# Optimization experiments

Hardware: AMD Instinct MI355X
Metric: run time of the kernel (lower is better)

The kernel has to match this reference:

```python
import jax, jax.numpy as jnp
import numpy as np

D_MODEL = 2048
N_HEADS = 16
HEAD_DIM = D_MODEL // N_HEADS  # 128
ROPE_BASE = 10000.0


def _rope_cos_sin(T, hd, dtype):
    inv_freq = 1.0 / (ROPE_BASE ** (jnp.arange(0, hd, 2, dtype=jnp.float32) / hd))
    freqs = jnp.arange(T, dtype=jnp.float32)[:, None] * inv_freq[None, :]  # [T, hd/2]
    emb = jnp.concatenate([freqs, freqs], axis=-1)  # [T, hd]
    return jnp.cos(emb).astype(dtype), jnp.sin(emb).astype(dtype)


def _rotate_half(x):
    h = x.shape[-1] // 2
    return jnp.concatenate([-x[..., h:], x[..., :h]], axis=-1)


def setup_inputs() -> dict:
    key = jax.random.key(0)
    k1, k2, k3, k4 = jax.random.split(key, 4)
    B, T = 2, 2048
    x = jax.random.normal(k1, (B, T, D_MODEL), dtype=jnp.float32)
    # Linear weights stored as [in, out] so y = x @ W (same math as torch's x @ W.T)
    Wqkv = jax.random.normal(k2, (D_MODEL, 3 * D_MODEL), dtype=jnp.float32) * (D_MODEL ** -0.5)
    Wproj = jax.random.normal(k3, (D_MODEL, D_MODEL), dtype=jnp.float32) * (D_MODEL ** -0.5)
    bproj = jax.random.normal(k4, (D_MODEL,), dtype=jnp.float32) * 0.01
    # additive causal mask: 0 on/below diagonal, -1e9 above
    causal = jnp.tril(jnp.ones((T, T), dtype=bool))
    mask = jnp.where(causal, 0.0, -1e9).astype(jnp.float32)
    return {"x": x, "Wqkv": Wqkv, "Wproj": Wproj, "bproj": bproj, "mask": mask}


def reference(x, Wqkv, Wproj, bproj, mask):
    B, T, D = x.shape
    H, hd = N_HEADS, HEAD_DIM
    scale = hd ** -0.5

    qkv = x @ Wqkv  # [B, T, 3D]
    q, k, v = jnp.split(qkv, 3, axis=-1)
    q = q.reshape(B, T, H, hd).transpose(0, 2, 1, 3)  # [B, H, T, hd]
    k = k.reshape(B, T, H, hd).transpose(0, 2, 1, 3)
    v = v.reshape(B, T, H, hd).transpose(0, 2, 1, 3)

    cos, sin = _rope_cos_sin(T, hd, x.dtype)  # [T, hd]
    q = q * cos + _rotate_half(q) * sin
    k = k * cos + _rotate_half(k) * sin

    attn = jnp.einsum('bhtd,bhsd->bhts', q, k) * scale  # [B, H, T, T]
    attn = attn + mask  # broadcast [T, T] over (B, H)
    attn = jax.nn.softmax(attn, axis=-1)
    out = jnp.einsum('bhts,bhsd->bhtd', attn, v)  # [B, H, T, hd]
    out = out.transpose(0, 2, 1, 3).reshape(B, T, D)
    return out @ Wproj + bproj
```

## Files before the change

### kernel.cpp

```cpp
#include <hip/hip_runtime.h>
#include <cstdint>

#define BB 2
#define TT 2048
#define DM 2048
#define NH 16
#define HD 128
#define QKVN 6144

using f32x4   = __attribute__((ext_vector_type(4))) float;
using bf16x8  = __attribute__((ext_vector_type(8))) __bf16;
using ushort8 = __attribute__((ext_vector_type(8))) unsigned short;

static __device__ __forceinline__ unsigned short f2bf(float f) {
    uint32_t u = __builtin_bit_cast(uint32_t, f);
    u += 0x7FFFu + ((u >> 16) & 1u);
    return (unsigned short)(u >> 16);
}
static __device__ __forceinline__ float bf2f(unsigned short h) {
    return __builtin_bit_cast(float, ((uint32_t)h) << 16);
}

#define GLOAD16(SRC, DST)                                               \
    __builtin_amdgcn_global_load_lds(                                   \
        (const __attribute__((address_space(1))) void*)(SRC),           \
        (__attribute__((address_space(3))) void*)(DST), 16, 0, 0)

__global__ __launch_bounds__(256) void k_split(const float* __restrict__ in,
                                               unsigned short* __restrict__ hi,
                                               unsigned short* __restrict__ lo,
                                               int n4) {
    int i = blockIdx.x * 256 + threadIdx.x;
    if (i >= n4) return;
    float4 v = reinterpret_cast<const float4*>(in)[i];
    ushort4 h, l;
    h.x = f2bf(v.x); l.x = f2bf(v.x - bf2f(h.x));
    h.y = f2bf(v.y); l.y = f2bf(v.y - bf2f(h.y));
    h.z = f2bf(v.z); l.z = f2bf(v.z - bf2f(h.z));
    h.w = f2bf(v.w); l.w = f2bf(v.w - bf2f(h.w));
    reinterpret_cast<ushort4*>(hi)[i] = h;
    reinterpret_cast<ushort4*>(lo)[i] = l;
}

__global__ __launch_bounds__(256) void k_tsplit(const float* __restrict__ W,
                                                unsigned short* __restrict__ th,
                                                int K, int N) {
    __shared__ float tile[32][33];
    int bn = blockIdx.x * 32, bk = blockIdx.y * 32;
    int tx = threadIdx.x, ty = threadIdx.y;
#pragma unroll
    for (int r = 0; r < 4; r++)
        tile[ty + 8 * r][tx] = W[(size_t)(bk + ty + 8 * r) * N + bn + tx];
    __syncthreads();
#pragma unroll
    for (int r = 0; r < 4; r++) {
        float v = tile[tx][ty + 8 * r];
        int row = bn + ty + 8 * r, col = bk + tx;
        th[(size_t)row * K + col] = f2bf(v);
    }
}

template <int EPI>
__global__ __launch_bounds__(512, 2) void k_gemm(
    const unsigned short* __restrict__ Ah, const unsigned short* __restrict__ Al,
    const unsigned short* __restrict__ Bh,
    unsigned short* __restrict__ Ch,
    float* __restrict__ Cf, const float* __restrict__ bias,
    int M, int N, int K) {
    __shared__ unsigned short sAh[2][16384];
    __shared__ unsigned short sAl[2][16384];
    __shared__ unsigned short sBh[2][8192];

    const int nwg = gridDim.x * gridDim.y;
    const int L = blockIdx.y * gridDim.x + blockIdx.x;
    const int logical = (L & 7) * (nwg >> 3) + (L >> 3);
    const int bx = logical % gridDim.x, by = logical / gridDim.x;

    const int tid = threadIdx.x;
    const int wave = tid >> 6, lane = tid & 63;
    const int g = lane >> 4, r16 = lane & 15;
    const int arow0 = by * 256, bcol0 = bx * 128;
    const int wr = (wave >> 1) * 64, wc = (wave & 1) * 64;
    const int sw8 = r16 & 7;

    const int srow = tid >> 3;
    const int scol = ((tid & 7) ^ (srow & 7)) << 3;

    f32x4 acc[4][4];
#pragma unroll
    for (int m = 0; m < 4; m++)
#pragma unroll
        for (int n = 0; n < 4; n++) acc[m][n] = (f32x4){0.f, 0.f, 0.f, 0.f};

    const int NT = K >> 6;

    auto stage = [&](int buf, int tk) {
        const size_t kof = (size_t)tk * 64 + scol;
#pragma unroll
        for (int i = 0; i < 4; i++) {
            size_t off = (size_t)(arow0 + i * 64 + srow) * K + kof;
            GLOAD16(Ah + off, &sAh[buf][(i * 512 + tid) * 8]);
            GLOAD16(Al + off, &sAl[buf][(i * 512 + tid) * 8]);
        }
#pragma unroll
        for (int i = 0; i < 2; i++) {
            size_t off = (size_t)(bcol0 + i * 64 + srow) * K + kof;
            GLOAD16(Bh + off, &sBh[buf][(i * 512 + tid) * 8]);
        }
    };

    stage(0, 0);
    asm volatile("s_waitcnt vmcnt(0)" ::: "memory");
    __builtin_amdgcn_s_barrier();

    int cur = 0;
    for (int t = 0; t < NT; ++t) {
        bf16x8 ah0[4], al0[4], bh0[4], ah1[4], al1[4], bh1[4];
#pragma unroll
        for (int m = 0; m < 4; m++) {
            int ro = (wr + m * 16 + r16) * 64 + ((g ^ sw8) << 3);
            ah0[m] = __builtin_bit_cast(bf16x8, *(const ushort8*)&sAh[cur][ro]);
            al0[m] = __builtin_bit_cast(bf16x8, *(const ushort8*)&sAl[cur][ro]);
        }
#pragma unroll
        for (int n = 0; n < 4; n++) {
            int ro = (wc + n * 16 + r16) * 64 + ((g ^ sw8) << 3);
            bh0[n] = __builtin_bit_cast(bf16x8, *(const ushort8*)&sBh[cur][ro]);
        }
        __builtin_amdgcn_sched_barrier(0);
        if (t + 1 < NT) stage(cur ^ 1, t + 1);
        __builtin_amdgcn_sched_barrier(0);
#pragma unroll
        for (int m = 0; m < 4; m++) {
            int ro = (wr + m * 16 + r16) * 64 + (((4 + g) ^ sw8) << 3);
            ah1[m] = __builtin_bit_cast(bf16x8, *(const ushort8*)&sAh[cur][ro]);
            al1[m] = __builtin_bit_cast(bf16x8, *(const ushort8*)&sAl[cur][ro]);
        }
#pragma unroll
        for (int n = 0; n < 4; n++) {
            int ro = (wc + n * 16 + r16) * 64 + (((4 + g) ^ sw8) << 3);
            bh1[n] = __builtin_bit_cast(bf16x8, *(const ushort8*)&sBh[cur][ro]);
        }
        __builtin_amdgcn_sched_barrier(0);
        asm volatile("s_waitcnt lgkmcnt(12)" ::: "memory");
        __builtin_amdgcn_sched_barrier(0);
        __builtin_amdgcn_s_setprio(1);
#pragma unroll
        for (int m = 0; m < 4; m++)
#pragma unroll
            for (int n = 0; n < 4; n++) {
                acc[m][n] = __builtin_amdgcn_mfma_f32_16x16x32_bf16(ah0[m], bh0[n], acc[m][n], 0, 0, 0);
                acc[m][n] = __builtin_amdgcn_mfma_f32_16x16x32_bf16(al0[m], bh0[n], acc[m][n], 0, 0, 0);
            }
        __builtin_amdgcn_s_setprio(0);
        asm volatile("s_waitcnt lgkmcnt(0)" ::: "memory");
        __builtin_amdgcn_sched_barrier(0);
        __builtin_amdgcn_s_setprio(1);
#pragma unroll
        for (int m = 0; m < 4; m++)
#pragma unroll
            for (int n = 0; n < 4; n++) {
                acc[m][n] = __builtin_amdgcn_mfma_f32_16x16x32_bf16(ah1[m], bh1[n], acc[m][n], 0, 0, 0);
                acc[m][n] = __builtin_amdgcn_mfma_f32_16x16x32_bf16(al1[m], bh1[n], acc[m][n], 0, 0, 0);
            }
        __builtin_amdgcn_s_setprio(0);
        asm volatile("s_waitcnt vmcnt(0)" ::: "memory");
        __builtin_amdgcn_s_barrier();
        cur ^= 1;
    }

#pragma unroll
    for (int m = 0; m < 4; m++)
#pragma unroll
        for (int n = 0; n < 4; n++) {
            int col = bcol0 + wc + n * 16 + r16;
#pragma unroll
            for (int j = 0; j < 4; j++) {
                int row = arow0 + wr + m * 16 + g * 4 + j;
                float v = acc[m][n][j];
                if (EPI == 0) {
                    Ch[(size_t)row * N + col] = f2bf(v);
                } else {
                    Cf[(size_t)row * N + col] = v + bias[col];
                }
            }
        }
}

__global__ __launch_bounds__(256) void k_rope(unsigned short* __restrict__ qh) {
    __shared__ float row[4096];
    __shared__ float cs[64], sn[64];
    const int rb = blockIdx.x;
    const int t = rb & (TT - 1);
    const int tid = threadIdx.x;
    if (tid < 64) {
        float invf = 1.0f / powf(10000.0f, (float)tid * (1.0f / 64.0f));
        float s, c;
        sincosf((float)t * invf, &s, &c);
        cs[tid] = c; sn[tid] = s;
    }
    const size_t base = (size_t)rb * QKVN;
#pragma unroll
    for (int i = 0; i < 2; i++) {
        int c0 = (tid + i * 256) * 8;
        ushort8 h = *(const ushort8*)&qh[base + c0];
#pragma unroll
        for (int e = 0; e < 8; e++) row[c0 + e] = bf2f(h[e]);
    }
    __syncthreads();
#pragma unroll
    for (int i = 0; i < 2; i++) {
        int c0 = (tid + i * 256) * 8;
        int d0 = c0 & 127;
        ushort8 h;
#pragma unroll
        for (int e = 0; e < 8; e++) {
            int c = c0 + e, d = d0 + e;
            float x = row[c];
            float xr = (d < 64) ? -row[c + 64] : row[c - 64];
            float v = x * cs[d & 63] + xr * sn[d & 63];
            h[e] = f2bf(v);
        }
        *(ushort8*)&qh[base + c0] = h;
    }
}

__global__ __launch_bounds__(128) void k_vt(const unsigned short* __restrict__ qkvh,
                                            unsigned short* __restrict__ vt) {
    const int bh = blockIdx.x;
    const int tc = blockIdx.y;
    const int d = threadIdx.x;
    const int b = bh >> 4, h = bh & 15;
    unsigned short buf[64];
    const size_t src0 = ((size_t)(b * TT + tc * 64)) * QKVN + 4096 + h * 128 + d;
#pragma unroll
    for (int ttt = 0; ttt < 64; ttt++) buf[ttt] = qkvh[src0 + (size_t)ttt * QKVN];
    const size_t dst = ((size_t)bh * 128 + d) * TT + tc * 64;
#pragma unroll
    for (int i = 0; i < 8; i++)
        *(ushort8*)&vt[dst + i * 8] = *(const ushort8*)&buf[i * 8];
}

__global__ __launch_bounds__(256) void k_flash(const unsigned short* __restrict__ qkvh,
                                               const unsigned short* __restrict__ vt,
                                               unsigned short* __restrict__ aoh,
                                               unsigned short* __restrict__ aol) {
    __shared__ unsigned short sK[2][64 * 128];
    __shared__ unsigned short sV[2][128 * 64];
    __shared__ unsigned short sP[4][16 * 64];

    const int L = blockIdx.y * gridDim.x + blockIdx.x;
    const int logical = (L & 7) * 128 + (L >> 3);
    const int bh = logical >> 5;
    const int qb = 31 - (logical & 31);
    const int b = bh >> 4, h = bh & 15;

    const int tid = threadIdx.x, wave = tid >> 6, lane = tid & 63;
    const int g = lane >> 4, r16 = lane & 15;
    const float scale = 0.08838834764831845f;

    bf16x8 qf[4];
    {
        const int qrow = qb * 64 + wave * 16 + r16;
        const size_t qbase = ((size_t)(b * TT) + qrow) * QKVN + h * 128;
#pragma unroll
        for (int kk = 0; kk < 4; kk++) {
            ushort8 u = *(const ushort8*)&qkvh[qbase + kk * 32 + g * 8];
            ushort8 o;
#pragma unroll
            for (int e = 0; e < 8; e++) o[e] = f2bf(bf2f(u[e]) * scale);
            qf[kk] = __builtin_bit_cast(bf16x8, o);
        }
    }

    f32x4 oacc[8];
#pragma unroll
    for (int n = 0; n < 8; n++) oacc[n] = (f32x4){0.f, 0.f, 0.f, 0.f};
    float mrun[4], lrun[4];
#pragma unroll
    for (int j = 0; j < 4; j++) { mrun[j] = -1e30f; lrun[j] = 0.f; }

    const int k_row_st = wave * 4 + (lane >> 4);
    const int v_row_st = wave * 8 + (lane >> 3);
    const int lidx = wave * 512 + lane * 8;

    auto stage = [&](int buf, int kb) {
#pragma unroll
        for (int i = 0; i < 4; i++) {
            int krow = i * 16 + k_row_st;
            int kcol = ((lane & 15) ^ (krow & 7)) << 3;
            GLOAD16(qkvh + ((size_t)(b * TT + kb * 64 + krow)) * QKVN + 2048 + h * 128 + kcol,
                    &sK[buf][i * 2048 + lidx]);
            int vrow = i * 32 + v_row_st;
            int vcol = ((lane & 7) ^ (vrow & 7)) << 3;
            GLOAD16(vt + ((size_t)bh * 128 + vrow) * TT + kb * 64 + vcol,
                    &sV[buf][i * 2048 + lidx]);
        }
    };

    const int nkb = qb + 1;
    int cur = 0;
    stage(0, 0);

    for (int kb = 0; kb < nkb; kb++) {
        __syncthreads();
        if (kb + 1 < nkb) stage(cur ^ 1, kb + 1);

        f32x4 sacc[4];
#pragma unroll
        for (int n = 0; n < 4; n++) sacc[n] = (f32x4){0.f, 0.f, 0.f, 0.f};
#pragma unroll
        for (int n = 0; n < 4; n++) {
            const int krow = n * 16 + r16;
            const int rbase = krow * 128;
            const int sw = krow & 7;
#pragma unroll
            for (int kk = 0; kk < 4; kk++) {
                int slot = (kk * 4 + g) ^ sw;
                bf16x8 kf = __builtin_bit_cast(bf16x8, *(const ushort8*)&sK[cur][rbase + slot * 8]);
                sacc[n] = __builtin_amdgcn_mfma_f32_16x16x32_bf16(qf[kk], kf, sacc[n], 0, 0, 0);
            }
        }

        const int key0 = kb * 64;
#pragma unroll
        for (int j = 0; j < 4; j++) {
            const int prow = g * 4 + j;
            const int qg = qb * 64 + wave * 16 + prow;
            float s0 = sacc[0][j], s1 = sacc[1][j], s2 = sacc[2][j], s3 = sacc[3][j];
            if (kb == qb) {
                if (key0 + r16 > qg)      s0 = -1e30f;
                if (key0 + 16 + r16 > qg) s1 = -1e30f;
                if (key0 + 32 + r16 > qg) s2 = -1e30f;
                if (key0 + 48 + r16 > qg) s3 = -1e30f;
            }
            float tmax = fmaxf(fmaxf(s0, s1), fmaxf(s2, s3));
#pragma unroll
            for (int off = 8; off >= 1; off >>= 1) tmax = fmaxf(tmax, __shfl_xor(tmax, off));
            float mnew = fmaxf(mrun[j], tmax);
            float corr = __expf(mrun[j] - mnew);
            float p0 = __expf(s0 - mnew), p1 = __expf(s1 - mnew);
            float p2 = __expf(s2 - mnew), p3 = __expf(s3 - mnew);
            float rs = (p0 + p1) + (p2 + p3);
#pragma unroll
            for (int off = 8; off >= 1; off >>= 1) rs += __shfl_xor(rs, off);
            lrun[j] = lrun[j] * corr + rs;
            mrun[j] = mnew;
#pragma unroll
            for (int n = 0; n < 8; n++) oacc[n][j] *= corr;
            const int pb = prow * 64, sw = prow & 7, e = r16 & 7, hi2 = (r16 >> 3);
            sP[wave][pb + (((0 + hi2) ^ sw) << 3) + e] = f2bf(p0);
            sP[wave][pb + (((2 + hi2) ^ sw) << 3) + e] = f2bf(p1);
            sP[wave][pb + (((4 + hi2) ^ sw) << 3) + e] = f2bf(p2);
            sP[wave][pb + (((6 + hi2) ^ sw) << 3) + e] = f2bf(p3);
        }

#pragma unroll
        for (int kk = 0; kk < 2; kk++) {
            const int slot = (kk * 4 + g) ^ (r16 & 7);
            bf16x8 pf = __builtin_bit_cast(bf16x8, *(const ushort8*)&sP[wave][r16 * 64 + slot * 8]);
#pragma unroll
            for (int n = 0; n < 8; n++) {
                const int d = n * 16 + r16;
                bf16x8 vf = __builtin_bit_cast(bf16x8, *(const ushort8*)&sV[cur][d * 64 + slot * 8]);
                oacc[n] = __builtin_amdgcn_mfma_f32_16x16x32_bf16(pf, vf, oacc[n], 0, 0, 0);
            }
        }
        cur ^= 1;
    }

#pragma unroll
    for (int j = 0; j < 4; j++) {
        float inv = 1.0f / lrun[j];
        int qg = qb * 64 + wave * 16 + g * 4 + j;
        size_t obase = ((size_t)(b * TT) + qg) * DM + h * 128;
#pragma unroll
        for (int n = 0; n < 8; n++) {
            float v = oacc[n][j] * inv;
            unsigned short hh = f2bf(v);
            aoh[obase + n * 16 + r16] = hh;
            aol[obase + n * 16 + r16] = f2bf(v - bf2f(hh));
        }
    }
}

extern "C" void kernel_launch(void* const* d_in, const int* in_sizes, int n_in,
                              void* d_out, int out_size, void* d_ws, size_t ws_size,
                              hipStream_t stream) {
    const float* x = (const float*)d_in[0];
    const float* Wqkv = (const float*)d_in[1];
    const float* Wproj = (const float*)d_in[2];
    const float* bproj = (const float*)d_in[3];

    uint8_t* w = (uint8_t*)d_ws;
    auto alloc = [&](size_t bytes) { uint8_t* p = w; w += bytes; return p; };
    unsigned short* xh   = (unsigned short*)alloc(8388608ull * 2);
    unsigned short* xl   = (unsigned short*)alloc(8388608ull * 2);
    unsigned short* wqh  = (unsigned short*)alloc(12582912ull * 2);
    unsigned short* wph  = (unsigned short*)alloc(4194304ull * 2);
    unsigned short* qkvh = (unsigned short*)alloc(25165824ull * 2);
    unsigned short* vtp  = (unsigned short*)alloc(8388608ull * 2);
    unsigned short* aoh  = (unsigned short*)alloc(8388608ull * 2);
    unsigned short* aol  = (unsigned short*)alloc(8388608ull * 2);

    k_split<<<dim3(8192), dim3(256), 0, stream>>>(x, xh, xl, 2097152);
    k_tsplit<<<dim3(192, 64), dim3(32, 8), 0, stream>>>(Wqkv, wqh, 2048, 6144);
    k_tsplit<<<dim3(64, 64), dim3(32, 8), 0, stream>>>(Wproj, wph, 2048, 2048);
    k_gemm<0><<<dim3(48, 16), dim3(512), 0, stream>>>(xh, xl, wqh,
                                                      qkvh, nullptr, nullptr,
                                                      4096, 6144, 2048);
    k_rope<<<dim3(4096), dim3(256), 0, stream>>>(qkvh);
    k_vt<<<dim3(32, 32), dim3(128), 0, stream>>>(qkvh, vtp);
    k_flash<<<dim3(32, 32), dim3(256), 0, stream>>>(qkvh, vtp, aoh, aol);
    k_gemm<1><<<dim3(16, 16), dim3(512), 0, stream>>>(aoh, aol, wph,
                                                      nullptr, (float*)d_out, bproj,
                                                      4096, 2048, 2048);
}
```

Before: 589.8 us.

## Interleave GEMM LDS reads, global prefetch and MFMA in four sub-phases

Splits each K-tile iteration of the split-bf16 GEMM into four sub-phases. Each sub-phase issues a subset of LDS fragment reads and one slice of the next tile's global-to-LDS prefetch (A-hi, A-lo, then B), then runs a quarter of the MFMAs, with workgroup barriers between phases. The goal is to overlap memory traffic with matrix math more evenly and to hold fewer fragments in registers at once. In exchange it adds three extra barriers per iteration and relies on hand-tuned lgkmcnt waits being correct.

```diff
diff --git a/kernel.cpp b/kernel.cpp
--- a/kernel.cpp
+++ b/kernel.cpp
@@ -67,9 +67,9 @@
     unsigned short* __restrict__ Ch,
     float* __restrict__ Cf, const float* __restrict__ bias,
     int M, int N, int K) {
-    __shared__ unsigned short sAh[2][16384];
-    __shared__ unsigned short sAl[2][16384];
-    __shared__ unsigned short sBh[2][8192];
+    __shared__ __align__(16) unsigned short sAh[2][16384];
+    __shared__ __align__(16) unsigned short sAl[2][16384];
+    __shared__ __align__(16) unsigned short sBh[2][8192];
 
     const int nwg = gridDim.x * gridDim.y;
     const int L = blockIdx.y * gridDim.x + blockIdx.x;
@@ -94,78 +94,120 @@
 
     const int NT = K >> 6;
 
-    auto stage = [&](int buf, int tk) {
+    auto stageA_hi = [&](int buf, int tk) {
         const size_t kof = (size_t)tk * 64 + scol;
 #pragma unroll
-        for (int i = 0; i < 4; i++) {
-            size_t off = (size_t)(arow0 + i * 64 + srow) * K + kof;
-            GLOAD16(Ah + off, &sAh[buf][(i * 512 + tid) * 8]);
-            GLOAD16(Al + off, &sAl[buf][(i * 512 + tid) * 8]);
-        }
-#pragma unroll
-        for (int i = 0; i < 2; i++) {
-            size_t off = (size_t)(bcol0 + i * 64 + srow) * K + kof;
-            GLOAD16(Bh + off, &sBh[buf][(i * 512 + tid) * 8]);
-        }
-    };
-
-    stage(0, 0);
-    asm volatile("s_waitcnt vmcnt(0)" ::: "memory");
-    __builtin_amdgcn_s_barrier();
+        for (int i = 0; i < 4; i++)
+            GLOAD16(Ah + (size_t)(arow0 + i * 64 + srow) * K + kof,
+                    &sAh[buf][(i * 512 + tid) * 8]);
+    };
+    auto stageA_lo = [&](int buf, int tk) {
+        const size_t kof = (size_t)tk * 64 + scol;
+#pragma unroll
+        for (int i = 0; i < 4; i++)
+            GLOAD16(Al + (size_t)(arow0 + i * 64 + srow) * K + kof,
+                    &sAl[buf][(i * 512 + tid) * 8]);
+    };
+    auto stageB = [&](int buf, int tk) {
+        const size_t kof = (size_t)tk * 64 + scol;
+#pragma unroll
+        for (int i = 0; i < 2; i++)
+            GLOAD16(Bh + (size_t)(bcol0 + i * 64 + srow) * K + kof,
+                    &sBh[buf][(i * 512 + tid) * 8]);
+    };
+
+    auto rdA = [&](int buf, int m, int co, bf16x8& h, bf16x8& l) {
+        int ro = (wr + m * 16 + r16) * 64 + co;
+        h = __builtin_bit_cast(bf16x8, *(const ushort8*)&sAh[buf][ro]);
+        l = __builtin_bit_cast(bf16x8, *(const ushort8*)&sAl[buf][ro]);
+    };
+    auto rdB = [&](int buf, int n, int co) {
+        int ro = (wc + n * 16 + r16) * 64 + co;
+        return __builtin_bit_cast(bf16x8, *(const ushort8*)&sBh[buf][ro]);
+    };
+
+    stageA_hi(0, 0); stageA_lo(0, 0); stageB(0, 0);
 
     int cur = 0;
     for (int t = 0; t < NT; ++t) {
+        asm volatile("s_waitcnt vmcnt(0)" ::: "memory");
+        __builtin_amdgcn_s_barrier();
+        const bool pf = (t + 1 < NT);
+        const int nb = cur ^ 1;
+        const int co0 = (g ^ sw8) << 3, co1 = ((4 + g) ^ sw8) << 3;
+
         bf16x8 ah0[4], al0[4], bh0[4], ah1[4], al1[4], bh1[4];
-#pragma unroll
-        for (int m = 0; m < 4; m++) {
-            int ro = (wr + m * 16 + r16) * 64 + ((g ^ sw8) << 3);
-            ah0[m] = __builtin_bit_cast(bf16x8, *(const ushort8*)&sAh[cur][ro]);
-            al0[m] = __builtin_bit_cast(bf16x8, *(const ushort8*)&sAl[cur][ro]);
-        }
-#pragma unroll
-        for (int n = 0; n < 4; n++) {
-            int ro = (wc + n * 16 + r16) * 64 + ((g ^ sw8) << 3);
-            bh0[n] = __builtin_bit_cast(bf16x8, *(const ushort8*)&sBh[cur][ro]);
-        }
-        __builtin_amdgcn_sched_barrier(0);
-        if (t + 1 < NT) stage(cur ^ 1, t + 1);
-        __builtin_amdgcn_sched_barrier(0);
-#pragma unroll
-        for (int m = 0; m < 4; m++) {
-            int ro = (wr + m * 16 + r16) * 64 + (((4 + g) ^ sw8) << 3);
-            ah1[m] = __builtin_bit_cast(bf16x8, *(const ushort8*)&sAh[cur][ro]);
-            al1[m] = __builtin_bit_cast(bf16x8, *(const ushort8*)&sAl[cur][ro]);
-        }
-#pragma unroll
-        for (int n = 0; n < 4; n++) {
-            int ro = (wc + n * 16 + r16) * 64 + (((4 + g) ^ sw8) << 3);
-            bh1[n] = __builtin_bit_cast(bf16x8, *(const ushort8*)&sBh[cur][ro]);
-        }
-        __builtin_amdgcn_sched_barrier(0);
-        asm volatile("s_waitcnt lgkmcnt(12)" ::: "memory");
+
+#pragma unroll
+        for (int n = 0; n < 4; n++) bh0[n] = rdB(cur, n, co0);
+        rdA(cur, 0, co0, ah0[0], al0[0]);
+        rdA(cur, 1, co0, ah0[1], al0[1]);
+        __builtin_amdgcn_sched_barrier(0);
+        rdA(cur, 2, co0, ah0[2], al0[2]);
+        rdA(cur, 3, co0, ah0[3], al0[3]);
+        __builtin_amdgcn_sched_barrier(0);
+        if (pf) stageA_hi(nb, t + 1);
+        asm volatile("s_waitcnt lgkmcnt(4)" ::: "memory");
         __builtin_amdgcn_sched_barrier(0);
         __builtin_amdgcn_s_setprio(1);
 #pragma unroll
-        for (int m = 0; m < 4; m++)
+        for (int m = 0; m < 2; m++)
 #pragma unroll
             for (int n = 0; n < 4; n++) {
                 acc[m][n] = __builtin_amdgcn_mfma_f32_16x16x32_bf16(ah0[m], bh0[n], acc[m][n], 0, 0, 0);
                 acc[m][n] = __builtin_amdgcn_mfma_f32_16x16x32_bf16(al0[m], bh0[n], acc[m][n], 0, 0, 0);
             }
         __builtin_amdgcn_s_setprio(0);
-        asm volatile("s_waitcnt lgkmcnt(0)" ::: "memory");
+        __builtin_amdgcn_s_barrier();
+
+        rdA(cur, 0, co1, ah1[0], al1[0]);
+        rdA(cur, 1, co1, ah1[1], al1[1]);
+        __builtin_amdgcn_sched_barrier(0);
+        if (pf) stageA_lo(nb, t + 1);
+        asm volatile("s_waitcnt lgkmcnt(4)" ::: "memory");
         __builtin_amdgcn_sched_barrier(0);
         __builtin_amdgcn_s_setprio(1);
 #pragma unroll
-        for (int m = 0; m < 4; m++)
+        for (int m = 2; m < 4; m++)
+#pragma unroll
+            for (int n = 0; n < 4; n++) {
+                acc[m][n] = __builtin_amdgcn_mfma_f32_16x16x32_bf16(ah0[m], bh0[n], acc[m][n], 0, 0, 0);
+                acc[m][n] = __builtin_amdgcn_mfma_f32_16x16x32_bf16(al0[m], bh0[n], acc[m][n], 0, 0, 0);
+            }
+        __builtin_amdgcn_s_setprio(0);
+        __builtin_amdgcn_s_barrier();
+
+#pragma unroll
+        for (int n = 0; n < 4; n++) bh1[n] = rdB(cur, n, co1);
+        __builtin_amdgcn_sched_barrier(0);
+        rdA(cur, 2, co1, ah1[2], al1[2]);
+        rdA(cur, 3, co1, ah1[3], al1[3]);
+        __builtin_amdgcn_sched_barrier(0);
+        if (pf) stageB(nb, t + 1);
+        asm volatile("s_waitcnt lgkmcnt(4)" ::: "memory");
+        __builtin_amdgcn_sched_barrier(0);
+        __builtin_amdgcn_s_setprio(1);
+#pragma unroll
+        for (int m = 0; m < 2; m++)
 #pragma unroll
             for (int n = 0; n < 4; n++) {
                 acc[m][n] = __builtin_amdgcn_mfma_f32_16x16x32_bf16(ah1[m], bh1[n], acc[m][n], 0, 0, 0);
                 acc[m][n] = __builtin_amdgcn_mfma_f32_16x16x32_bf16(al1[m], bh1[n], acc[m][n], 0, 0, 0);
             }
         __builtin_amdgcn_s_setprio(0);
-        asm volatile("s_waitcnt vmcnt(0)" ::: "memory");
         __builtin_amdgcn_s_barrier();
+
+        asm volatile("s_waitcnt lgkmcnt(0)" ::: "memory");
+        __builtin_amdgcn_sched_barrier(0);
+        __builtin_amdgcn_s_setprio(1);
+#pragma unroll
+        for (int m = 2; m < 4; m++)
+#pragma unroll
+            for (int n = 0; n < 4; n++) {
+                acc[m][n] = __builtin_amdgcn_mfma_f32_16x16x32_bf16(ah1[m], bh1[n], acc[m][n], 0, 0, 0);
+                acc[m][n] = __builtin_amdgcn_mfma_f32_16x16x32_bf16(al1[m], bh1[n], acc[m][n], 0, 0, 0);
+            }
+        __builtin_amdgcn_s_setprio(0);
         cur ^= 1;
     }
 
```

Result: faster. 559.6 us (-5.1%).
